# Optimization experiments

Measured on AMD Instinct MI355X. Metric: run time of the kernel, lower is better.

The kernel has to match this reference:

```python
import jax, jax.numpy as jnp
import numpy as np

V, D, DEPTH, L, H, DH, FF = 32000, 1024, 4, 2048, 16, 64, 4096
INNER = H * DH
EPS = 1e-5


def ln(x, g, b):
    m = jnp.mean(x, axis=-1, keepdims=True)
    v = jnp.mean(jnp.square(x - m), axis=-1, keepdims=True)
    return (x - m) * jax.lax.rsqrt(v + EPS) * g + b


def setup_inputs() -> dict:
    key = jax.random.key(0)
    ks = jax.random.split(key, 16)
    s = 0.02
    inp = {
        'x': jax.random.randint(ks[0], (1, L), 0, V),
        'tok_emb': jax.random.normal(ks[1], (V, D), jnp.float32) * s,
        'pos_emb': jax.random.normal(ks[2], (L, D), jnp.float32) * s,
        'attn_ng': jnp.ones((DEPTH, D), jnp.float32),
        'attn_nb': jnp.zeros((DEPTH, D), jnp.float32),
        'wqkv': jax.random.normal(ks[3], (DEPTH, D, 3 * INNER), jnp.float32) * s,
        'wo': jax.random.normal(ks[4], (DEPTH, INNER, D), jnp.float32) * s,
        'bo': jnp.zeros((DEPTH, D), jnp.float32),
        'out_ng': jnp.ones((DEPTH, D), jnp.float32),
        'out_nb': jnp.zeros((DEPTH, D), jnp.float32),
        'ff_ng': jnp.ones((DEPTH, D), jnp.float32),
        'ff_nb': jnp.zeros((DEPTH, D), jnp.float32),
        'w1': jax.random.normal(ks[5], (DEPTH, D, FF), jnp.float32) * s,
        'b1': jnp.zeros((DEPTH, FF), jnp.float32),
        'w2': jax.random.normal(ks[6], (DEPTH, FF, D), jnp.float32) * s,
        'b2': jnp.zeros((DEPTH, D), jnp.float32),
        'fin_g': jnp.ones((D,), jnp.float32),
        'fin_b': jnp.zeros((D,), jnp.float32),
        'w_logit': jax.random.normal(ks[7], (D, V), jnp.float32) * s,
        'b_logit': jnp.zeros((V,), jnp.float32),
    }
    return inp


def reference(x, tok_emb, pos_emb, attn_ng, attn_nb, wqkv, wo, bo, out_ng, out_nb,
              ff_ng, ff_nb, w1, b1, w2, b2, fin_g, fin_b, w_logit, b_logit):
    n = x.shape[1]
    scale = DH ** -0.5
    # causal keep-mask: j <= i (lower triangular incl diagonal)
    causal = jnp.tril(jnp.ones((n, n), bool))
    h = tok_emb[x] + pos_emb[:n][None]  # [b, n, D]
    for l in range(DEPTH):
        # --- ReLA attention ---
        y = ln(h, attn_ng[l], attn_nb[l])
        qkv = y @ wqkv[l]  # [b, n, 3*INNER]
        q, k, v = jnp.split(qkv, 3, axis=-1)
        q = q.reshape(-1, n, H, DH).transpose(0, 2, 1, 3) * scale  # [b,H,n,d]
        k = k.reshape(-1, n, H, DH).transpose(0, 2, 1, 3)
        v = v.reshape(-1, n, H, DH).transpose(0, 2, 1, 3)
        sim = jnp.einsum('bhid,bhjd->bhij', q, k)
        attn = jnp.where(causal, jax.nn.relu(sim), 0.0)  # mask then ReLU
        o = jnp.einsum('bhij,bhjd->bhid', attn, v)
        o = o.transpose(0, 2, 1, 3).reshape(-1, n, INNER)  # [b,n,INNER]
        o = ln(o @ wo[l] + bo[l], out_ng[l], out_nb[l])
        h = o + h
        # --- FFN ---
        y = ln(h, ff_ng[l], ff_nb[l])
        y = jax.nn.gelu(y @ w1[l] + b1[l], approximate=False) @ w2[l] + b2[l]
        h = y + h
    return ln(h, fin_g, fin_b) @ w_logit + b_logit
```

## Files before the change

### kernel.cpp

```cpp
#include <hip/hip_runtime.h>
#include <hip/hip_bf16.h>
#include <math.h>

#define SEQ   2048
#define DM    1024
#define NH    16
#define DHD   64
#define FFD   4096
#define NV    32000

typedef __bf16 bf16x8 __attribute__((ext_vector_type(8)));
typedef float  f32x4  __attribute__((ext_vector_type(4)));

typedef __attribute__((address_space(1))) void* gas_ptr;
typedef __attribute__((address_space(3))) void* las_ptr;

static __device__ __forceinline__ void gload16(const void* g, void* l) {
  __builtin_amdgcn_global_load_lds((gas_ptr)g, (las_ptr)l, 16, 0, 0);
}

static __device__ __forceinline__ unsigned short f2bf(float f) {
  unsigned int x = __float_as_uint(f);
  return (unsigned short)((x + 0x7fffu + ((x >> 16) & 1u)) >> 16);
}

static __device__ __forceinline__ bf16x8 ld_frag(const unsigned short* p) {
  union { uint4 u; bf16x8 v; } r;
  r.u = *(const uint4*)p;
  return r.v;
}

__global__ __launch_bounds__(256)
void k_transpose_bf16(const float* __restrict__ in, unsigned short* __restrict__ out,
                      int K, int N, size_t lstride) {
  in  += (size_t)blockIdx.z * lstride;
  out += (size_t)blockIdx.z * lstride;
  __shared__ float tl[64 * 65];
  const int bk = blockIdx.x * 64, bn = blockIdx.y * 64;
  const int t = threadIdx.x;
  const int tx = t & 15, ty = t >> 4;
#pragma unroll
  for (int i = 0; i < 4; ++i) {
    const int r = i * 16 + ty;
    float4 v = *(const float4*)&in[(size_t)(bk + r) * N + bn + tx * 4];
    tl[(tx * 4 + 0) * 65 + r] = v.x;
    tl[(tx * 4 + 1) * 65 + r] = v.y;
    tl[(tx * 4 + 2) * 65 + r] = v.z;
    tl[(tx * 4 + 3) * 65 + r] = v.w;
  }
  __syncthreads();
#pragma unroll
  for (int j = 0; j < 2; ++j) {
    const int f = j * 256 + t;
    const int n = f >> 3, kc = (f & 7) * 8;
    union { unsigned short u[8]; uint4 v; } pk;
#pragma unroll
    for (int e = 0; e < 8; ++e) pk.u[e] = f2bf(tl[n * 65 + kc + e]);
    *(uint4*)&out[(size_t)(bn + n) * K + bk + kc] = pk.v;
  }
}

__global__ __launch_bounds__(256)
void k_vT(const unsigned short* __restrict__ qkv, unsigned short* __restrict__ vT) {
  __shared__ unsigned short tile[32][33];
  const int bs = blockIdx.x * 32, bd = blockIdx.y * 32;
  const int tx = threadIdx.x & 31, ty = threadIdx.x >> 5;
#pragma unroll
  for (int r = ty; r < 32; r += 8)
    tile[r][tx] = qkv[(size_t)(bs + r) * (3 * DM) + 2 * DM + bd + tx];
  __syncthreads();
#pragma unroll
  for (int r = ty; r < 32; r += 8)
    vT[(size_t)(bd + r) * SEQ + bs + tx] = tile[tx][r];
}

__global__ __launch_bounds__(256)
void k_embed(const int* __restrict__ x, const float* __restrict__ tok,
             const float* __restrict__ pos, float* __restrict__ h) {
  const int row = blockIdx.x;
  const int d = threadIdx.x * 4;
  const int tk = x[row];
  float4 a = *(const float4*)(tok + (size_t)tk * DM + d);
  float4 p = *(const float4*)(pos + (size_t)row * DM + d);
  float4 o; o.x = a.x + p.x; o.y = a.y + p.y; o.z = a.z + p.z; o.w = a.w + p.w;
  *(float4*)(h + (size_t)row * DM + d) = o;
}

__global__ __launch_bounds__(256)
void k_ln_bf16(const float* __restrict__ in, const float* __restrict__ g,
               const float* __restrict__ b, unsigned short* __restrict__ out) {
  const int row = blockIdx.x, t = threadIdx.x;
  float4 v = *(const float4*)(in + (size_t)row * DM + t * 4);
  float s = v.x + v.y + v.z + v.w;
  float q = v.x * v.x + v.y * v.y + v.z * v.z + v.w * v.w;
#pragma unroll
  for (int o = 32; o; o >>= 1) { s += __shfl_xor(s, o); q += __shfl_xor(q, o); }
  __shared__ float ls[4], lq[4];
  if ((t & 63) == 0) { ls[t >> 6] = s; lq[t >> 6] = q; }
  __syncthreads();
  s = ls[0] + ls[1] + ls[2] + ls[3];
  q = lq[0] + lq[1] + lq[2] + lq[3];
  const float mean = s * (1.f / DM);
  const float rstd = rsqrtf(q * (1.f / DM) - mean * mean + 1e-5f);
  float4 gg = *(const float4*)(g + t * 4);
  float4 bb = *(const float4*)(b + t * 4);
  ushort4 o4;
  o4.x = f2bf((v.x - mean) * rstd * gg.x + bb.x);
  o4.y = f2bf((v.y - mean) * rstd * gg.y + bb.y);
  o4.z = f2bf((v.z - mean) * rstd * gg.z + bb.z);
  o4.w = f2bf((v.w - mean) * rstd * gg.w + bb.w);
  *(ushort4*)(out + (size_t)row * DM + t * 4) = o4;
}

__global__ __launch_bounds__(256)
void k_ored(const float* __restrict__ sl, unsigned short* __restrict__ obf) {
  const int row = blockIdx.x, t = threadIdx.x;
  const size_t idx = (size_t)row * DM + t * 4;
  float4 a = *(const float4*)(sl + idx);
  float4 b = *(const float4*)(sl + (size_t)SEQ * DM + idx);
  ushort4 o4;
  o4.x = f2bf(a.x + b.x);
  o4.y = f2bf(a.y + b.y);
  o4.z = f2bf(a.z + b.z);
  o4.w = f2bf(a.w + b.w);
  *(ushort4*)(obf + idx) = o4;
}

__global__ __launch_bounds__(256)
void k_addslab_ln_ln(float* __restrict__ h, const float* __restrict__ sl,
                     const float* __restrict__ bo,
                     const float* __restrict__ g1, const float* __restrict__ b1,
                     const float* __restrict__ g2, const float* __restrict__ b2,
                     unsigned short* __restrict__ out) {
  const int row = blockIdx.x, t = threadIdx.x;
  __shared__ float ls[4], lq[4], ls2[4], lq2[4];
  const size_t idx = (size_t)row * DM + t * 4;
  float4 v = *(const float4*)(bo + t * 4);
#pragma unroll
  for (int c = 0; c < 4; ++c) {
    float4 p = *(const float4*)(sl + (size_t)c * SEQ * DM + idx);
    v.x += p.x; v.y += p.y; v.z += p.z; v.w += p.w;
  }
  float s = v.x + v.y + v.z + v.w;
  float q = v.x * v.x + v.y * v.y + v.z * v.z + v.w * v.w;
#pragma unroll
  for (int o = 32; o; o >>= 1) { s += __shfl_xor(s, o); q += __shfl_xor(q, o); }
  if ((t & 63) == 0) { ls[t >> 6] = s; lq[t >> 6] = q; }
  __syncthreads();
  s = ls[0] + ls[1] + ls[2] + ls[3];
  q = lq[0] + lq[1] + lq[2] + lq[3];
  const float mean = s * (1.f / DM);
  const float rstd = rsqrtf(q * (1.f / DM) - mean * mean + 1e-5f);
  float4 gg = *(const float4*)(g1 + t * 4);
  float4 bb = *(const float4*)(b1 + t * 4);
  float4 hv = *(const float4*)(h + idx);
  hv.x += (v.x - mean) * rstd * gg.x + bb.x;
  hv.y += (v.y - mean) * rstd * gg.y + bb.y;
  hv.z += (v.z - mean) * rstd * gg.z + bb.z;
  hv.w += (v.w - mean) * rstd * gg.w + bb.w;
  *(float4*)(h + idx) = hv;
  float s2 = hv.x + hv.y + hv.z + hv.w;
  float q2 = hv.x * hv.x + hv.y * hv.y + hv.z * hv.z + hv.w * hv.w;
#pragma unroll
  for (int o = 32; o; o >>= 1) { s2 += __shfl_xor(s2, o); q2 += __shfl_xor(q2, o); }
  if ((t & 63) == 0) { ls2[t >> 6] = s2; lq2[t >> 6] = q2; }
  __syncthreads();
  s2 = ls2[0] + ls2[1] + ls2[2] + ls2[3];
  q2 = lq2[0] + lq2[1] + lq2[2] + lq2[3];
  const float mean2 = s2 * (1.f / DM);
  const float rstd2 = rsqrtf(q2 * (1.f / DM) - mean2 * mean2 + 1e-5f);
  float4 g2v = *(const float4*)(g2 + t * 4);
  float4 b2v = *(const float4*)(b2 + t * 4);
  ushort4 o4;
  o4.x = f2bf((hv.x - mean2) * rstd2 * g2v.x + b2v.x);
  o4.y = f2bf((hv.y - mean2) * rstd2 * g2v.y + b2v.y);
  o4.z = f2bf((hv.z - mean2) * rstd2 * g2v.z + b2v.z);
  o4.w = f2bf((hv.w - mean2) * rstd2 * g2v.w + b2v.w);
  *(ushort4*)(out + (size_t)row * DM + t * 4) = o4;
}

__global__ __launch_bounds__(256)
void k_redadd_ln(float* __restrict__ h, const float* __restrict__ sl,
                 const float* __restrict__ b2,
                 const float* __restrict__ g, const float* __restrict__ b,
                 unsigned short* __restrict__ out) {
  const int row = blockIdx.x, t = threadIdx.x;
  __shared__ float ls[4], lq[4];
  const size_t idx = (size_t)row * DM + t * 4;
  float4 hv = *(const float4*)(h + idx);
  float4 bb = *(const float4*)(b2 + t * 4);
  hv.x += bb.x; hv.y += bb.y; hv.z += bb.z; hv.w += bb.w;
#pragma unroll
  for (int c = 0; c < 4; ++c) {
    float4 p = *(const float4*)(sl + (size_t)c * SEQ * DM + idx);
    hv.x += p.x; hv.y += p.y; hv.z += p.z; hv.w += p.w;
  }
  *(float4*)(h + idx) = hv;
  float s = hv.x + hv.y + hv.z + hv.w;
  float q = hv.x * hv.x + hv.y * hv.y + hv.z * hv.z + hv.w * hv.w;
#pragma unroll
  for (int o = 32; o; o >>= 1) { s += __shfl_xor(s, o); q += __shfl_xor(q, o); }
  if ((t & 63) == 0) { ls[t >> 6] = s; lq[t >> 6] = q; }
  __syncthreads();
  s = ls[0] + ls[1] + ls[2] + ls[3];
  q = lq[0] + lq[1] + lq[2] + lq[3];
  const float mean = s * (1.f / DM);
  const float rstd = rsqrtf(q * (1.f / DM) - mean * mean + 1e-5f);
  float4 gg = *(const float4*)(g + t * 4);
  float4 b1 = *(const float4*)(b + t * 4);
  ushort4 o4;
  o4.x = f2bf((hv.x - mean) * rstd * gg.x + b1.x);
  o4.y = f2bf((hv.y - mean) * rstd * gg.y + b1.y);
  o4.z = f2bf((hv.z - mean) * rstd * gg.z + b1.z);
  o4.w = f2bf((hv.w - mean) * rstd * gg.w + b1.w);
  *(ushort4*)(out + (size_t)row * DM + t * 4) = o4;
}

template<int EPI>
__global__ __launch_bounds__(256)
void k_gemm4(const unsigned short* __restrict__ A, const unsigned short* __restrict__ Bt,
             float* __restrict__ outF, unsigned short* __restrict__ outB,
             const float* __restrict__ bias, int N, int K, int kLen, int gm) {
  __shared__ __align__(16) unsigned short L[16384];
  const int nwg = gridDim.x, pid = blockIdx.x;
  const int qq = nwg >> 3, rr = nwg & 7;
  const int xcd = pid & 7, lo = pid >> 3;
  const int wg = ((xcd < rr) ? xcd * (qq + 1) : rr * (qq + 1) + (xcd - rr) * qq) + lo;
  const int bm = wg % gm, bn = wg / gm;
  const int kOff = blockIdx.y * kLen;
  const int t = threadIdx.x, lane = t & 63, w = t >> 6;
  const int wm = w >> 1, wn = w & 1, lr = lane & 15, lg = lane >> 4;

  const unsigned short* gA[2]; const unsigned short* gB[2];
  unsigned short* lA[2]; unsigned short* lB[2];
#pragma unroll
  for (int j = 0; j < 2; ++j) {
    const int f = j * 256 + t;
    const int row = f >> 2;
    const int c = (f & 3) ^ ((row >> 1) & 3);
    gA[j] = A  + (size_t)(bm * 128 + row) * K + kOff + c * 8;
    gB[j] = Bt + (size_t)(bn * 128 + row) * K + kOff + c * 8;
    lA[j] = L + f * 8;
    lB[j] = L + 4096 + f * 8;
  }
  auto stage = [&](int k0, int cb) {
#pragma unroll
    for (int j = 0; j < 2; ++j) gload16(gA[j] + k0, lA[j] + cb * 8192);
#pragma unroll
    for (int j = 0; j < 2; ++j) gload16(gB[j] + k0, lB[j] + cb * 8192);
  };

  int offA[4], offB[4];
#pragma unroll
  for (int mt = 0; mt < 4; ++mt) {
    const int rowA = wm * 64 + mt * 16 + lr;
    offA[mt] = rowA * 32 + ((lg ^ ((rowA >> 1) & 3)) << 3);
    const int rowB = wn * 64 + mt * 16 + lr;
    offB[mt] = 4096 + rowB * 32 + ((lg ^ ((rowB >> 1) & 3)) << 3);
  }

  f32x4 acc[4][4];
#pragma unroll
  for (int i = 0; i < 4; ++i)
#pragma unroll
    for (int j = 0; j < 4; ++j) acc[i][j] = (f32x4){0.f, 0.f, 0.f, 0.f};

  const int NT = kLen >> 5;
  stage(0, 0);
  stage(32, 1);

  for (int tt = 0; tt < NT; ++tt) {
    const int cb = tt & 1;
    if (tt + 1 < NT) asm volatile("s_waitcnt vmcnt(4)" ::: "memory");
    else             asm volatile("s_waitcnt vmcnt(0)" ::: "memory");
    __builtin_amdgcn_s_barrier();
    const unsigned short* buf = L + cb * 8192;
    bf16x8 af[4], bfr[4];
#pragma unroll
    for (int mt = 0; mt < 4; ++mt) {
      af[mt]  = ld_frag(buf + offA[mt]);
      bfr[mt] = ld_frag(buf + offB[mt]);
    }
    __builtin_amdgcn_s_setprio(1);
#pragma unroll
    for (int mt = 0; mt < 4; ++mt)
#pragma unroll
      for (int nt = 0; nt < 4; ++nt)
        acc[mt][nt] = __builtin_amdgcn_mfma_f32_16x16x32_bf16(af[mt], bfr[nt], acc[mt][nt], 0, 0, 0);
    __builtin_amdgcn_s_setprio(0);
    __builtin_amdgcn_s_barrier();
    if (tt + 2 < NT) stage((tt + 2) << 5, cb);
  }

  const int rbase = bm * 128 + wm * 64;
  const int cbase = bn * 128 + wn * 64;
  float* outP = outF;
  if constexpr (EPI == 4) outP = outF + (size_t)blockIdx.y * SEQ * N;
#pragma unroll
  for (int mt = 0; mt < 4; ++mt) {
#pragma unroll
    for (int nt = 0; nt < 4; ++nt) {
      const int col = cbase + nt * 16 + lr;
      float bv = 0.f;
      if constexpr (EPI == 1 || EPI == 2) bv = bias[col];
#pragma unroll
      for (int r = 0; r < 4; ++r) {
        const int row = rbase + mt * 16 + lg * 4 + r;
        float v = acc[mt][nt][r] + bv;
        if constexpr (EPI == 2) v = 0.5f * v * (1.f + erff(v * 0.70710678118f));
        if constexpr (EPI == 0 || EPI == 2) outB[(size_t)row * N + col] = f2bf(v);
        else                                outP[(size_t)row * N + col] = v;
      }
    }
  }
}

__global__ __launch_bounds__(256)
void k_rela_attn(const unsigned short* __restrict__ qkv,
                 const unsigned short* __restrict__ vT,
                 float* __restrict__ osl) {
  const int jb = blockIdx.x;
  const int hd = blockIdx.y;
  const int z  = blockIdx.z;
  const int qbA = jb, qbB = 31 - jb;
  const int ha = (qbA + 2) >> 1, hb = (qbB + 2) >> 1;
  const int t = threadIdx.x, lane = t & 63, w = t >> 6;
  const int lr = lane & 15, lg = lane >> 4;

  __shared__ __align__(16) unsigned short Qs[128 * 64];
  __shared__ __align__(16) unsigned short Ks[2][64 * 64];
  __shared__ __align__(16) unsigned short Vs[2][64 * 64];
  __shared__ __align__(16) unsigned short Ps[4][16 * 72];

  const int sr8 = lane >> 3;
  const int sch = ((lane & 7) ^ sr8) << 3;

#pragma unroll
  for (int qi = 0; qi < 4; ++qi) {
    const int i = w * 4 + qi;
    const int rl = i * 8 + sr8;
    const int grow = (rl < 64) ? (qbA * 64 + rl) : (qbB * 64 + rl - 64);
    gload16(qkv + (size_t)grow * (3 * DM) + hd * DHD + sch, Qs + i * 512);
  }
  __syncthreads();

  bf16x8 qfA[2], qfB[2];
#pragma unroll
  for (int ks = 0; ks < 2; ++ks) {
    const int rowA = w * 16 + lr;
    qfA[ks] = ld_frag(&Qs[rowA * 64 + (((ks * 4 + lg) ^ (lr & 7)) << 3)]);
    const int rowB = 64 + w * 16 + lr;
    qfB[ks] = ld_frag(&Qs[rowB * 64 + (((ks * 4 + lg) ^ (lr & 7)) << 3)]);
  }

  const f32x4 zero = {0.f, 0.f, 0.f, 0.f};
  f32x4 accA[4], accB[4];
#pragma unroll
  for (int nt = 0; nt < 4; ++nt) { accA[nt] = zero; accB[nt] = zero; }

  auto stage = [&](int kt, int cb) {
#pragma unroll
    for (int qi = 0; qi < 2; ++qi) {
      const int i = w * 2 + qi;
      const int rl = i * 8 + sr8;
      gload16(qkv + (size_t)(kt * 64 + rl) * (3 * DM) + DM + hd * DHD + sch, &Ks[cb][i * 512]);
      gload16(vT + (size_t)(hd * DHD + rl) * SEQ + kt * 64 + sch, &Vs[cb][i * 512]);
    }
  };

  auto tile_step = [&](const bf16x8* qf, f32x4* acc, int qb, int kt, int cb) {
    f32x4 sv[4];
#pragma unroll
    for (int nt = 0; nt < 4; ++nt) sv[nt] = zero;
#pragma unroll
    for (int ks = 0; ks < 2; ++ks)
#pragma unroll
      for (int nt = 0; nt < 4; ++nt) {
        bf16x8 kf = ld_frag(&Ks[cb][(nt * 16 + lr) * 64 + (((ks * 4 + lg) ^ (lr & 7)) << 3)]);
        sv[nt] = __builtin_amdgcn_mfma_f32_16x16x32_bf16(qf[ks], kf, sv[nt], 0, 0, 0);
      }
    const bool diag = (kt == qb);
#pragma unroll
    for (int nt = 0; nt < 4; ++nt)
#pragma unroll
      for (int r = 0; r < 4; ++r) {
        float v = fmaxf(sv[nt][r], 0.f) * 0.125f;
        if (diag) {
          const int ii = w * 16 + lg * 4 + r;
          const int jj = nt * 16 + lr;
          if (jj > ii) v = 0.f;
        }
        Ps[w][(lg * 4 + r) * 72 + nt * 16 + lr] = f2bf(v);
      }
#pragma unroll
    for (int ks = 0; ks < 2; ++ks) {
      bf16x8 pf = ld_frag(&Ps[w][lr * 72 + ks * 32 + lg * 8]);
#pragma unroll
      for (int nt = 0; nt < 4; ++nt) {
        bf16x8 vf = ld_frag(&Vs[cb][(nt * 16 + lr) * 64 + (((ks * 4 + lg) ^ (lr & 7)) << 3)]);
        acc[nt] = __builtin_amdgcn_mfma_f32_16x16x32_bf16(pf, vf, acc[nt], 0, 0, 0);
      }
    }
  };

  auto run = [&](int beg, int end, int mode) {
    if (beg >= end) return;
    stage(beg, 0);
    for (int kt = beg; kt < end; ++kt) {
      const int cb = (kt - beg) & 1;
      if (kt + 1 < end) {
        stage(kt + 1, cb ^ 1);
        asm volatile("s_waitcnt vmcnt(4)" ::: "memory");
      } else {
        asm volatile("s_waitcnt vmcnt(0)" ::: "memory");
      }
      __builtin_amdgcn_s_barrier();
      if (mode != 1) tile_step(qfB, accB, qbB, kt, cb);
      if (mode == 1 || (mode == 0 && kt < ha)) tile_step(qfA, accA, qbA, kt, cb);
      __builtin_amdgcn_s_barrier();
    }
  };

  if (z == 0) {
    run(0, hb, 0);
  } else {
    run(ha, qbA + 1, 1);
    run(hb, qbB + 1, 2);
  }

  float* op = osl + (size_t)z * SEQ * DM;
#pragma unroll
  for (int nt = 0; nt < 4; ++nt)
#pragma unroll
    for (int r = 0; r < 4; ++r) {
      const int col = hd * DHD + nt * 16 + lr;
      const int rowA = qbA * 64 + w * 16 + lg * 4 + r;
      op[(size_t)rowA * DM + col] = accA[nt][r];
      const int rowB = qbB * 64 + w * 16 + lg * 4 + r;
      op[(size_t)rowB * DM + col] = accB[nt][r];
    }
}

extern "C" void kernel_launch(void* const* d_in, const int* in_sizes, int n_in,
                              void* d_out, int out_size, void* d_ws, size_t ws_size,
                              hipStream_t stream) {
  const int*   x       = (const int*)d_in[0];
  const float* tok_emb = (const float*)d_in[1];
  const float* pos_emb = (const float*)d_in[2];
  const float* attn_ng = (const float*)d_in[3];
  const float* attn_nb = (const float*)d_in[4];
  const float* wqkv    = (const float*)d_in[5];
  const float* wo      = (const float*)d_in[6];
  const float* bo      = (const float*)d_in[7];
  const float* out_ng  = (const float*)d_in[8];
  const float* out_nb  = (const float*)d_in[9];
  const float* ff_ng   = (const float*)d_in[10];
  const float* ff_nb   = (const float*)d_in[11];
  const float* w1      = (const float*)d_in[12];
  const float* b1      = (const float*)d_in[13];
  const float* w2      = (const float*)d_in[14];
  const float* b2      = (const float*)d_in[15];
  const float* fin_g   = (const float*)d_in[16];
  const float* fin_b   = (const float*)d_in[17];
  const float* w_logit = (const float*)d_in[18];
  const float* b_logit = (const float*)d_in[19];
  float* out = (float*)d_out;

  char* ws = (char*)d_ws;
  size_t off = 0;
  auto alloc = [&](size_t bytes) -> void* {
    void* p = ws + off;
    off = (off + bytes + 255) & ~(size_t)255;
    return p;
  };
  unsigned short* wqkvT = (unsigned short*)alloc(4ull * 3072 * 1024 * 2);
  unsigned short* woT   = (unsigned short*)alloc(4ull * 1024 * 1024 * 2);
  unsigned short* w1T   = (unsigned short*)alloc(4ull * 4096 * 1024 * 2);
  unsigned short* w2T   = (unsigned short*)alloc(4ull * 1024 * 4096 * 2);
  unsigned short* wlogT = (unsigned short*)alloc((size_t)NV * 1024 * 2);
  float*          h     = (float*)alloc((size_t)SEQ * DM * 4);
  unsigned short* ybf   = (unsigned short*)alloc((size_t)SEQ * DM * 2);
  unsigned short* qkvbf = (unsigned short*)alloc((size_t)SEQ * 3 * DM * 2);
  unsigned short* vTb   = (unsigned short*)alloc((size_t)DM * SEQ * 2);
  unsigned short* obf   = (unsigned short*)alloc((size_t)SEQ * DM * 2);
  unsigned short* ffbf  = (unsigned short*)alloc((size_t)SEQ * FFD * 2);
  float*          slabs = (float*)alloc(4ull * SEQ * DM * 4);
  (void)ws_size; (void)in_sizes; (void)n_in; (void)out_size;

  const dim3 B(256);

  k_transpose_bf16<<<dim3(16, 48, 4), B, 0, stream>>>(wqkv, wqkvT, 1024, 3072, (size_t)1024 * 3072);
  k_transpose_bf16<<<dim3(16, 16, 4), B, 0, stream>>>(wo, woT, 1024, 1024, (size_t)1024 * 1024);
  k_transpose_bf16<<<dim3(16, 64, 4), B, 0, stream>>>(w1, w1T, 1024, 4096, (size_t)1024 * 4096);
  k_transpose_bf16<<<dim3(64, 16, 4), B, 0, stream>>>(w2, w2T, 4096, 1024, (size_t)4096 * 1024);
  k_transpose_bf16<<<dim3(16, 500, 1), B, 0, stream>>>(w_logit, wlogT, 1024, NV, 0);

  k_embed<<<SEQ, B, 0, stream>>>(x, tok_emb, pos_emb, h);
  k_ln_bf16<<<SEQ, B, 0, stream>>>(h, attn_ng, attn_nb, ybf);

  for (int l = 0; l < 4; ++l) {
    k_gemm4<0><<<dim3(384), B, 0, stream>>>(
        ybf, wqkvT + (size_t)l * 3072 * 1024, nullptr, qkvbf, nullptr, 3072, 1024, 1024, 16);
    k_vT<<<dim3(SEQ / 32, DM / 32), B, 0, stream>>>(qkvbf, vTb);
    k_rela_attn<<<dim3(16, NH, 2), B, 0, stream>>>(qkvbf, vTb, slabs);
    k_ored<<<SEQ, B, 0, stream>>>(slabs, obf);
    k_gemm4<4><<<dim3(128, 4), B, 0, stream>>>(
        obf, woT + (size_t)l * 1024 * 1024, slabs, nullptr, nullptr, 1024, 1024, 256, 16);
    k_addslab_ln_ln<<<SEQ, B, 0, stream>>>(h, slabs, bo + l * DM,
                                           out_ng + l * DM, out_nb + l * DM,
                                           ff_ng + l * DM, ff_nb + l * DM, ybf);
    k_gemm4<2><<<dim3(512), B, 0, stream>>>(
        ybf, w1T + (size_t)l * 4096 * 1024, nullptr, ffbf, b1 + l * FFD, 4096, 1024, 1024, 16);
    k_gemm4<4><<<dim3(128, 4), B, 0, stream>>>(
        ffbf, w2T + (size_t)l * 1024 * 4096, slabs, nullptr, nullptr, 1024, 4096, 1024, 16);
    const float* ng = (l < 3) ? (attn_ng + (l + 1) * DM) : fin_g;
    const float* nb = (l < 3) ? (attn_nb + (l + 1) * DM) : fin_b;
    k_redadd_ln<<<SEQ, B, 0, stream>>>(h, slabs, b2 + l * DM, ng, nb, ybf);
  }

  k_gemm4<1><<<dim3(4000), B, 0, stream>>>(ybf, wlogT, out, nullptr, b_logit, NV, 1024, 1024, 16);
}
```

Measured before the change: 1.025 ms.

## Add 256x256-tile 8-wave GEMM with interleaved LDS pipeline for logits

Adds a new GEMM kernel that uses 256x256 output tiles, 512 threads, a 64 KB double-buffered LDS layout and XCD-aware workgroup remapping. Global-to-LDS staging of the next K tile is interleaved with quarter-tile MFMA groups, coordinated by explicit waitcnt and barriers. The final vocabulary projection now uses this kernel instead of the 128x128 gemm4. The goals are more data reuse per tile, fewer workgroups, and better overlap of loads with math. The cost is heavy register and LDS use, which may limit occupancy, and the fragile hand-tuned wait counts.

```diff
diff --git a/kernel.cpp b/kernel.cpp
--- a/kernel.cpp
+++ b/kernel.cpp
@@ -311,6 +311,137 @@
         if constexpr (EPI == 0 || EPI == 2) outB[(size_t)row * N + col] = f2bf(v);
         else                                outP[(size_t)row * N + col] = v;
       }
+    }
+  }
+}
+
+__global__ __launch_bounds__(512, 2)
+void k_gemm7(const unsigned short* __restrict__ A, const unsigned short* __restrict__ Bt,
+             float* __restrict__ outF, const float* __restrict__ bias,
+             int N, int K, int gm) {
+  __shared__ __align__(16) unsigned short L[65536];
+  const int nwg = gridDim.x, pid = blockIdx.x;
+  const int qq = nwg >> 3, rr = nwg & 7;
+  const int xcd = pid & 7, lo = pid >> 3;
+  const int wg = ((xcd < rr) ? xcd * (qq + 1) : rr * (qq + 1) + (xcd - rr) * qq) + lo;
+  const int bm = wg % gm, bn = wg / gm;
+  const int t = threadIdx.x, lane = t & 63, w = t >> 6;
+  const int wm = w >> 2, wn = w & 3, lr = lane & 15, lg = lane >> 4;
+  const int NT = K >> 6;
+
+  const unsigned short* gA = A  + (size_t)(bm * 256) * K;
+  const unsigned short* gB = Bt + (size_t)(bn * 256) * K;
+  const int rowLow = t >> 3;
+  const int colOff = ((t & 7) ^ ((t >> 3) & 7)) << 3;
+  const unsigned short* pA = gA + (size_t)rowLow * K + colOff;
+  const unsigned short* pB = gB + (size_t)rowLow * K + colOff;
+  unsigned short* const ldst = L + t * 8;
+
+  auto stageQ = [&](int which, int s, int q) {
+    const int ss = (s < NT) ? s : (NT - 1);
+    const unsigned short* g = (which ? pB : pA) + (size_t)(q * 64) * K + (ss << 6);
+    gload16(g, ldst + ((s & 1) << 15) + (which << 14) + (q << 12));
+  };
+
+  const int swz0 = ((0 + lg) ^ (lr & 7)) << 3;
+  const int swz1 = ((4 + lg) ^ (lr & 7)) << 3;
+  const int aBase = (wm * 128 + lr) * 64;
+  const int bBase = 16384 + (wn * 64 + lr) * 64;
+
+  f32x4 acc[8][4];
+#pragma unroll
+  for (int i = 0; i < 8; ++i)
+#pragma unroll
+    for (int j = 0; j < 4; ++j) acc[i][j] = (f32x4){0.f, 0.f, 0.f, 0.f};
+  bf16x8 af0[4][2], af1[4][2], bf0[2][2], bf1[2][2];
+
+  stageQ(0, 0, 0); stageQ(0, 0, 1); stageQ(0, 0, 2); stageQ(0, 0, 3);
+  stageQ(1, 0, 0); stageQ(1, 0, 1); stageQ(1, 0, 2); stageQ(1, 0, 3);
+  stageQ(0, 1, 0); stageQ(0, 1, 2); stageQ(1, 1, 0); stageQ(1, 1, 1);
+  stageQ(0, 1, 1); stageQ(0, 1, 3);
+  asm volatile("s_waitcnt vmcnt(6)" ::: "memory");
+  __builtin_amdgcn_s_barrier();
+#pragma unroll
+  for (int mt = 0; mt < 4; ++mt) {
+    af0[mt][0] = ld_frag(L + aBase + mt * 1024 + swz0);
+    af0[mt][1] = ld_frag(L + aBase + mt * 1024 + swz1);
+  }
+#pragma unroll
+  for (int n2 = 0; n2 < 2; ++n2) {
+    bf0[n2][0] = ld_frag(L + bBase + n2 * 1024 + swz0);
+    bf0[n2][1] = ld_frag(L + bBase + n2 * 1024 + swz1);
+  }
+
+#define MM(AF, BF, RB, CB)                                                        \
+  __builtin_amdgcn_s_setprio(1);                                                  \
+  _Pragma("unroll") for (int mt = 0; mt < 4; ++mt)                                \
+  _Pragma("unroll") for (int n2 = 0; n2 < 2; ++n2)                                \
+  _Pragma("unroll") for (int ks = 0; ks < 2; ++ks)                                \
+    acc[(RB) + mt][(CB) + n2] = __builtin_amdgcn_mfma_f32_16x16x32_bf16(          \
+        AF[mt][ks], BF[n2][ks], acc[(RB) + mt][(CB) + n2], 0, 0, 0);              \
+  __builtin_amdgcn_s_setprio(0);
+
+#define GROUP(BUF, NBUF, TT)                                                      \
+                                    \
+  stageQ(1, (TT) + 1, 2); stageQ(1, (TT) + 1, 3);                                 \
+  __builtin_amdgcn_s_barrier();                                                   \
+  _Pragma("unroll") for (int n2 = 0; n2 < 2; ++n2) {                              \
+    bf1[n2][0] = ld_frag(L + (BUF) + bBase + 2048 + n2 * 1024 + swz0);            \
+    bf1[n2][1] = ld_frag(L + (BUF) + bBase + 2048 + n2 * 1024 + swz1);            \
+  }                                                                               \
+  asm volatile("s_waitcnt lgkmcnt(4)" ::: "memory");                              \
+  MM(af0, bf0, 0, 0)                                                              \
+  __builtin_amdgcn_s_barrier();                                                   \
+                                    \
+  stageQ(0, (TT) + 2, 0); stageQ(0, (TT) + 2, 2);                                 \
+  __builtin_amdgcn_s_barrier();                                                   \
+  _Pragma("unroll") for (int mt = 0; mt < 4; ++mt) {                              \
+    af1[mt][0] = ld_frag(L + (BUF) + aBase + 4096 + mt * 1024 + swz0);            \
+    af1[mt][1] = ld_frag(L + (BUF) + aBase + 4096 + mt * 1024 + swz1);            \
+  }                                                                               \
+  asm volatile("s_waitcnt lgkmcnt(8)" ::: "memory");                              \
+  MM(af0, bf1, 0, 2)                                                              \
+  __builtin_amdgcn_s_barrier();                                                   \
+                                                \
+  stageQ(1, (TT) + 2, 0); stageQ(1, (TT) + 2, 1);                                 \
+  __builtin_amdgcn_s_barrier();                                                   \
+  asm volatile("s_waitcnt lgkmcnt(0)" ::: "memory");                              \
+  MM(af1, bf0, 4, 0)                                                              \
+  __builtin_amdgcn_s_barrier();                                                   \
+               \
+  stageQ(0, (TT) + 2, 1); stageQ(0, (TT) + 2, 3);                                 \
+  asm volatile("s_waitcnt vmcnt(6)" ::: "memory");                                \
+  __builtin_amdgcn_s_barrier();                                                   \
+  _Pragma("unroll") for (int mt = 0; mt < 4; ++mt) {                              \
+    af0[mt][0] = ld_frag(L + (NBUF) + aBase + mt * 1024 + swz0);                  \
+    af0[mt][1] = ld_frag(L + (NBUF) + aBase + mt * 1024 + swz1);                  \
+  }                                                                               \
+  _Pragma("unroll") for (int n2 = 0; n2 < 2; ++n2) {                              \
+    bf0[n2][0] = ld_frag(L + (NBUF) + bBase + n2 * 1024 + swz0);                  \
+    bf0[n2][1] = ld_frag(L + (NBUF) + bBase + n2 * 1024 + swz1);                  \
+  }                                                                               \
+  asm volatile("s_waitcnt lgkmcnt(12)" ::: "memory");                             \
+  MM(af1, bf1, 4, 2)                                                              \
+  __builtin_amdgcn_s_barrier();
+
+  for (int i = 0; i < (NT >> 1); ++i) {
+    const int T0 = 2 * i, T1 = 2 * i + 1;
+    GROUP(0, 32768, T0)
+    GROUP(32768, 0, T1)
+  }
+#undef GROUP
+#undef MM
+
+#pragma unroll
+  for (int ai = 0; ai < 8; ++ai) {
+    const int row0 = bm * 256 + wm * 128 + (ai >> 2) * 64 + (ai & 3) * 16 + lg * 4;
+#pragma unroll
+    for (int bj = 0; bj < 4; ++bj) {
+      const int col = bn * 256 + wn * 64 + (bj >> 1) * 32 + (bj & 1) * 16 + lr;
+      const float bv = bias[col];
+#pragma unroll
+      for (int r = 0; r < 4; ++r)
+        outF[(size_t)(row0 + r) * N + col] = acc[ai][bj][r] + bv;
     }
   }
 }
@@ -488,6 +619,7 @@
   (void)ws_size; (void)in_sizes; (void)n_in; (void)out_size;
 
   const dim3 B(256);
+  const dim3 G7(512);
 
   k_transpose_bf16<<<dim3(16, 48, 4), B, 0, stream>>>(wqkv, wqkvT, 1024, 3072, (size_t)1024 * 3072);
   k_transpose_bf16<<<dim3(16, 16, 4), B, 0, stream>>>(wo, woT, 1024, 1024, (size_t)1024 * 1024);
@@ -518,5 +650,5 @@
     k_redadd_ln<<<SEQ, B, 0, stream>>>(h, slabs, b2 + l * DM, ng, nb, ybf);
   }
 
-  k_gemm4<1><<<dim3(4000), B, 0, stream>>>(ybf, wlogT, out, nullptr, b_logit, NV, 1024, 1024, 16);
-}
+  k_gemm7<<<dim3(1000), G7, 0, stream>>>(ybf, wlogT, out, b_logit, NV, 1024, 8);
+}
```

After: 1.046 ms. 1.02x slower.

## Drop split-K attention partitioning and write bf16 output directly from attention

Applied to the files above, without the earlier changes.

Replaces the two-way key-range split of the ReLA attention kernel (fp32 partial slabs plus a separate reduction kernel) with a single block per query-pair and head that iterates the whole causal range and stores bf16 output. This removes a kernel launch and the fp32 partial write/read traffic. In exchange the attention grid halves, lowering parallelism and occupancy while lengthening each block.

```diff
diff --git a/kernel.cpp b/kernel.cpp
--- a/kernel.cpp
+++ b/kernel.cpp
@@ -110,20 +110,6 @@
   o4.z = f2bf((v.z - mean) * rstd * gg.z + bb.z);
   o4.w = f2bf((v.w - mean) * rstd * gg.w + bb.w);
   *(ushort4*)(out + (size_t)row * DM + t * 4) = o4;
-}
-
-__global__ __launch_bounds__(256)
-void k_ored(const float* __restrict__ sl, unsigned short* __restrict__ obf) {
-  const int row = blockIdx.x, t = threadIdx.x;
-  const size_t idx = (size_t)row * DM + t * 4;
-  float4 a = *(const float4*)(sl + idx);
-  float4 b = *(const float4*)(sl + (size_t)SEQ * DM + idx);
-  ushort4 o4;
-  o4.x = f2bf(a.x + b.x);
-  o4.y = f2bf(a.y + b.y);
-  o4.z = f2bf(a.z + b.z);
-  o4.w = f2bf(a.w + b.w);
-  *(ushort4*)(obf + idx) = o4;
 }
 
 __global__ __launch_bounds__(256)
@@ -318,12 +304,10 @@
 __global__ __launch_bounds__(256)
 void k_rela_attn(const unsigned short* __restrict__ qkv,
                  const unsigned short* __restrict__ vT,
-                 float* __restrict__ osl) {
+                 unsigned short* __restrict__ obf) {
   const int jb = blockIdx.x;
   const int hd = blockIdx.y;
-  const int z  = blockIdx.z;
   const int qbA = jb, qbB = 31 - jb;
-  const int ha = (qbA + 2) >> 1, hb = (qbB + 2) >> 1;
   const int t = threadIdx.x, lane = t & 63, w = t >> 6;
   const int lr = lane & 15, lg = lane >> 4;
 
@@ -403,41 +387,30 @@
     }
   };
 
-  auto run = [&](int beg, int end, int mode) {
-    if (beg >= end) return;
-    stage(beg, 0);
-    for (int kt = beg; kt < end; ++kt) {
-      const int cb = (kt - beg) & 1;
-      if (kt + 1 < end) {
-        stage(kt + 1, cb ^ 1);
-        asm volatile("s_waitcnt vmcnt(4)" ::: "memory");
-      } else {
-        asm volatile("s_waitcnt vmcnt(0)" ::: "memory");
-      }
-      __builtin_amdgcn_s_barrier();
-      if (mode != 1) tile_step(qfB, accB, qbB, kt, cb);
-      if (mode == 1 || (mode == 0 && kt < ha)) tile_step(qfA, accA, qbA, kt, cb);
-      __builtin_amdgcn_s_barrier();
-    }
-  };
-
-  if (z == 0) {
-    run(0, hb, 0);
-  } else {
-    run(ha, qbA + 1, 1);
-    run(hb, qbB + 1, 2);
-  }
-
-  float* op = osl + (size_t)z * SEQ * DM;
+  stage(0, 0);
+  for (int kt = 0; kt <= qbB; ++kt) {
+    const int cb = kt & 1;
+    if (kt < qbB) {
+      stage(kt + 1, cb ^ 1);
+      asm volatile("s_waitcnt vmcnt(4)" ::: "memory");
+    } else {
+      asm volatile("s_waitcnt vmcnt(0)" ::: "memory");
+    }
+    __builtin_amdgcn_s_barrier();
+    tile_step(qfB, accB, qbB, kt, cb);
+    if (kt <= qbA) tile_step(qfA, accA, qbA, kt, cb);
+    __builtin_amdgcn_s_barrier();
+  }
+
 #pragma unroll
   for (int nt = 0; nt < 4; ++nt)
 #pragma unroll
     for (int r = 0; r < 4; ++r) {
       const int col = hd * DHD + nt * 16 + lr;
       const int rowA = qbA * 64 + w * 16 + lg * 4 + r;
-      op[(size_t)rowA * DM + col] = accA[nt][r];
+      obf[(size_t)rowA * DM + col] = f2bf(accA[nt][r]);
       const int rowB = qbB * 64 + w * 16 + lg * 4 + r;
-      op[(size_t)rowB * DM + col] = accB[nt][r];
+      obf[(size_t)rowB * DM + col] = f2bf(accB[nt][r]);
     }
 }
 
@@ -502,8 +475,7 @@
     k_gemm4<0><<<dim3(384), B, 0, stream>>>(
         ybf, wqkvT + (size_t)l * 3072 * 1024, nullptr, qkvbf, nullptr, 3072, 1024, 1024, 16);
     k_vT<<<dim3(SEQ / 32, DM / 32), B, 0, stream>>>(qkvbf, vTb);
-    k_rela_attn<<<dim3(16, NH, 2), B, 0, stream>>>(qkvbf, vTb, slabs);
-    k_ored<<<SEQ, B, 0, stream>>>(slabs, obf);
+    k_rela_attn<<<dim3(16, NH), B, 0, stream>>>(qkvbf, vTb, obf);
     k_gemm4<4><<<dim3(128, 4), B, 0, stream>>>(
         obf, woT + (size_t)l * 1024 * 1024, slabs, nullptr, nullptr, 1024, 1024, 256, 16);
     k_addslab_ln_ln<<<SEQ, B, 0, stream>>>(h, slabs, bo + l * DM,
```

After: 1.058 ms. 3.2% more time.
